# Kernel tuning notes

Measured on AMD Instinct MI355X. Metric: run time of the kernel, lower is better.

The kernel has to match this reference:

```python
import jax, jax.numpy as jnp
import numpy as np

B, L, D, H = 2, 2048, 1024, 16
DK = D // H


def setup_inputs() -> dict:
    key = jax.random.key(0)
    ks = jax.random.split(key, 13)
    s = 1.0 / np.sqrt(D)
    return {
        "q": jax.random.normal(ks[0], (B, L, D), jnp.float32),
        "k": jax.random.normal(ks[1], (B, L, D), jnp.float32),
        "v": jax.random.normal(ks[2], (B, L, D), jnp.float32),
        "mask": jax.random.randint(ks[3], (B, L, L), 0, 2, jnp.int32),
        "Wq": jax.random.normal(ks[4], (D, D), jnp.float32) * s,
        "bq": jnp.zeros((D,), jnp.float32),
        "Wk": jax.random.normal(ks[5], (D, D), jnp.float32) * s,
        "bk": jnp.zeros((D,), jnp.float32),
        "Wv": jax.random.normal(ks[6], (D, D), jnp.float32) * s,
        "bv": jnp.zeros((D,), jnp.float32),
        "Wo": jax.random.normal(ks[7], (D, D), jnp.float32) * s,
        "bo": jnp.zeros((D,), jnp.float32),
    }


def reference(q, k, v, mask, Wq, bq, Wk, bk, Wv, bv, Wo, bo):
    # projections: [B, L, D] -> [B, L, H, DK]
    qh = (q @ Wq + bq).reshape(B, L, H, DK)
    kh = (k @ Wk + bk).reshape(B, L, H, DK)
    vh = (v @ Wv + bv).reshape(B, L, H, DK)
    # scores scaled by d_model (module passes model_dim=d_model, not sqrt(d_k))
    attn = jnp.einsum("bqhd,bkhd->bhqk", qh, kh) / D
    attn = jnp.where(mask[:, None, :, :] == 0, jnp.float32(-1e9), attn)
    attn = jax.nn.softmax(attn, axis=-1)  # [B, H, Lq, Lk]
    ctx = jnp.einsum("bhqk,bkhd->bqhd", attn, vh)  # [B, Lq, H, DK]
    out = ctx.reshape(B, L, D) @ Wo + bo
    # original returns attn flattened head-major: [H*B, Lq, Lk]
    attn_out = attn.transpose(1, 0, 2, 3).reshape(H * B, L, L)
    return out, attn_out
```

## Files before the change

kernel.cpp:

```cpp
#include <hip/hip_runtime.h>
#include <cstdint>

typedef unsigned short u16;
typedef unsigned long long u64;
typedef __attribute__((ext_vector_type(8))) short short8;
typedef __attribute__((ext_vector_type(4))) float floatx4;

#define DEV __device__ __forceinline__

#define GLD16(gp, lp)                                                          \
  __builtin_amdgcn_global_load_lds(                                            \
      (const __attribute__((address_space(1))) void*)(gp),                     \
      (__attribute__((address_space(3))) void*)(lp), 16, 0, 0)

DEV u16 f2bf(float f) {
  union { float f; uint32_t u; } x; x.f = f;
  uint32_t r = x.u + 0x7fffu + ((x.u >> 16) & 1u);
  return (u16)(r >> 16);
}


__global__ __launch_bounds__(256) void cvt_bf16(
    const float* __restrict__ src, u16* __restrict__ dst) {
  int i = (blockIdx.x * 256 + threadIdx.x) * 4;
  float4 v = *(const float4*)(src + i);
  ushort4 o;
  o.x = f2bf(v.x); o.y = f2bf(v.y); o.z = f2bf(v.z); o.w = f2bf(v.w);
  *(ushort4*)(dst + i) = o;
}

__global__ __launch_bounds__(256) void pack_mask(
    const int* __restrict__ mask, u64* __restrict__ mw) {
  const int lane = threadIdx.x & 63;
  int gw = (blockIdx.x * 256 + threadIdx.x) >> 6;
  const int nwaves = (gridDim.x * 256) >> 6;
  const int total = (2 * 2048 * 2048) / 64;
  for (int c = gw; c < total; c += nwaves) {
    int v = mask[(size_t)c * 64 + lane];
    u64 b = __ballot(v != 0);
    if (lane == 0) mw[c] = b;
  }
}

__global__ __launch_bounds__(256) void transpose_w(
    const float* __restrict__ s0, const float* __restrict__ s1,
    const float* __restrict__ s2, const float* __restrict__ s3,
    u16* __restrict__ d0, u16* __restrict__ d1,
    u16* __restrict__ d2, u16* __restrict__ d3) {
  const float* S; u16* D;
  switch (blockIdx.z) {
    case 0: S = s0; D = d0; break;
    case 1: S = s1; D = d1; break;
    case 2: S = s2; D = d2; break;
    default: S = s3; D = d3; break;
  }
  __shared__ u16 t[64][68];
  const int tid = threadIdx.x;
  const int r0 = blockIdx.y * 64, c0 = blockIdx.x * 64;
#pragma unroll
  for (int i = 0; i < 4; ++i) {
    int idx = i * 256 + tid;
    int r = idx >> 4, c = (idx & 15) * 4;
    float4 v = *(const float4*)(S + (size_t)(r0 + r) * 1024 + c0 + c);
    t[r][c] = f2bf(v.x); t[r][c + 1] = f2bf(v.y);
    t[r][c + 2] = f2bf(v.z); t[r][c + 3] = f2bf(v.w);
  }
  __syncthreads();
#pragma unroll
  for (int i = 0; i < 4; ++i) {
    int idx = i * 256 + tid;
    int r = idx >> 4, c = (idx & 15) * 4;
    ushort4 v;
    v.x = t[c][r]; v.y = t[c + 1][r]; v.z = t[c + 2][r]; v.w = t[c + 3][r];
    *(ushort4*)(D + (size_t)(c0 + r) * 1024 + r0 + c) = v;
  }
}

__global__ __launch_bounds__(256) void gemm128(
    const u16* __restrict__ X, const u16* __restrict__ Wt,
    const float* __restrict__ bias, u16* __restrict__ outb,
    float* __restrict__ outf, int mode) {
  __shared__ __align__(16) u16 As[128 * 32];
  __shared__ __align__(16) u16 Bs[128 * 32];
  const int tid = threadIdx.x;
  const int wave = tid >> 6, lane = tid & 63;
  const int quad = lane >> 4, l16 = lane & 15;
  const int wm = (wave >> 1) * 64, wn = (wave & 1) * 64;
  const int m0 = blockIdx.x * 128, n0 = blockIdx.y * 128;

  floatx4 acc[4][4];
#pragma unroll
  for (int i = 0; i < 4; ++i)
#pragma unroll
    for (int j = 0; j < 4; ++j) acc[i][j] = (floatx4){0.f, 0.f, 0.f, 0.f};

  for (int k0 = 0; k0 < 1024; k0 += 32) {
#pragma unroll
    for (int r = 0; r < 2; ++r) {
      int c = r * 256 + tid;
      int row = c >> 2, off = (c & 3) * 8;
      GLD16(X + (size_t)(m0 + row) * 1024 + k0 + off, As + c * 8);
      GLD16(Wt + (size_t)(n0 + row) * 1024 + k0 + off, Bs + c * 8);
    }
    __syncthreads();
    short8 a[4], b[4];
#pragma unroll
    for (int i = 0; i < 4; ++i)
      a[i] = *(const short8*)(As + (wm + i * 16 + l16) * 32 + quad * 8);
#pragma unroll
    for (int i = 0; i < 4; ++i)
      b[i] = *(const short8*)(Bs + (wn + i * 16 + l16) * 32 + quad * 8);
#pragma unroll
    for (int mi = 0; mi < 4; ++mi)
#pragma unroll
      for (int ni = 0; ni < 4; ++ni)
        acc[mi][ni] = __builtin_amdgcn_mfma_f32_16x16x32_bf16(
            a[mi], b[ni], acc[mi][ni], 0, 0, 0);
    __syncthreads();
  }

#pragma unroll
  for (int mi = 0; mi < 4; ++mi) {
#pragma unroll
    for (int ni = 0; ni < 4; ++ni) {
      const int gn = n0 + wn + ni * 16 + l16;
      const float bv = bias[gn];
#pragma unroll
      for (int reg = 0; reg < 4; ++reg) {
        const int gm = m0 + wm + mi * 16 + quad * 4 + reg;
        const float v = acc[mi][ni][reg] + bv;
        if (mode == 2) {
          outf[(size_t)gm * 1024 + gn] = v;
        } else {
          int bb = gm >> 11, l = gm & 2047, hh = gn >> 6, dk = gn & 63;
          size_t addr = (mode == 0)
              ? (((size_t)(bb * 16 + hh) * 2048 + l) * 64 + dk)
              : (((size_t)(bb * 16 + hh) * 64 + dk) * 2048 + l);
          outb[addr] = f2bf(v);
        }
      }
    }
  }
}

__global__ __launch_bounds__(256) void rowsum_k(
    const u16* __restrict__ qh, const u16* __restrict__ kh,
    const u64* __restrict__ mw, float* __restrict__ rowinv) {
  const int tid = threadIdx.x;
  const int wave = tid >> 6, lane = tid & 63;
  const int quad = lane >> 4, l16 = lane & 15;
  const int q0 = blockIdx.x * 64, h = blockIdx.y, b = blockIdx.z;
  const int bh = b * 16 + h;

  __shared__ __align__(16) u16 Qs[64 * 72];
  __shared__ __align__(16) u16 Ks[128 * 72];
  __shared__ float red[4][64];

  const u16* qbase = qh + ((size_t)bh * 2048 + q0) * 64;
  const u16* kbase = kh + (size_t)bh * 2048 * 64;
  const u64* mwrow = mw + ((size_t)b * 2048 + q0) * 32;

#pragma unroll
  for (int r = 0; r < 2; ++r) {
    int c = r * 256 + tid;
    int row = c >> 3, off = (c & 7) * 8;
    uint4 v = *(const uint4*)(qbase + (size_t)c * 8);
    *(uint4*)(Qs + row * 72 + off) = v;
  }

  float rs[4][4];
#pragma unroll
  for (int i = 0; i < 4; ++i)
#pragma unroll
    for (int j = 0; j < 4; ++j) rs[i][j] = 0.f;

  for (int kt = 0; kt < 16; ++kt) {
#pragma unroll
    for (int r = 0; r < 4; ++r) {
      int c = r * 256 + tid;
      int row = c >> 3, off = (c & 7) * 8;
      uint4 v = *(const uint4*)(kbase + (size_t)kt * 8192 + c * 8);
      *(uint4*)(Ks + row * 72 + off) = v;
    }
    __syncthreads();

    floatx4 s[4][2];
#pragma unroll
    for (int i = 0; i < 4; ++i) {
      s[i][0] = (floatx4){0.f, 0.f, 0.f, 0.f};
      s[i][1] = (floatx4){0.f, 0.f, 0.f, 0.f};
    }
#pragma unroll
    for (int kk = 0; kk < 64; kk += 32) {
      short8 a[4], bb[2];
#pragma unroll
      for (int i = 0; i < 4; ++i)
        a[i] = *(const short8*)(Qs + (i * 16 + l16) * 72 + kk + quad * 8);
#pragma unroll
      for (int j = 0; j < 2; ++j)
        bb[j] = *(const short8*)(Ks + (wave * 32 + j * 16 + l16) * 72 + kk + quad * 8);
#pragma unroll
      for (int mi = 0; mi < 4; ++mi)
#pragma unroll
        for (int ni = 0; ni < 2; ++ni)
          s[mi][ni] = __builtin_amdgcn_mfma_f32_16x16x32_bf16(
              a[mi], bb[ni], s[mi][ni], 0, 0, 0);
    }
#pragma unroll
    for (int mi = 0; mi < 4; ++mi)
#pragma unroll
      for (int reg = 0; reg < 4; ++reg) {
        int row = mi * 16 + quad * 4 + reg;
        u64 w = mwrow[row * 32 + kt * 2 + (wave >> 1)];
#pragma unroll
        for (int ni = 0; ni < 2; ++ni) {
          int bit = (wave & 1) * 32 + ni * 16 + l16;
          float sv = s[mi][ni][reg] * (1.0f / 1024.0f);
          rs[mi][reg] += ((w >> bit) & 1) ? __expf(sv) : 0.f;
        }
      }
    __syncthreads();
  }

#pragma unroll
  for (int mi = 0; mi < 4; ++mi)
#pragma unroll
    for (int reg = 0; reg < 4; ++reg) {
      float v = rs[mi][reg];
      v += __shfl_xor(v, 1, 64);
      v += __shfl_xor(v, 2, 64);
      v += __shfl_xor(v, 4, 64);
      v += __shfl_xor(v, 8, 64);
      rs[mi][reg] = v;
    }
  if (l16 == 0) {
#pragma unroll
    for (int mi = 0; mi < 4; ++mi)
#pragma unroll
      for (int reg = 0; reg < 4; ++reg)
        red[wave][mi * 16 + quad * 4 + reg] = rs[mi][reg];
  }
  __syncthreads();
  if (tid < 64) {
    float sum = red[0][tid] + red[1][tid] + red[2][tid] + red[3][tid];
    rowinv[(size_t)bh * 2048 + q0 + tid] = (sum > 0.f) ? (1.0f / sum) : -1.0f;
  }
}

__global__ __launch_bounds__(256) void attn_k(
    const u16* __restrict__ qh, const u16* __restrict__ kh,
    const u16* __restrict__ vt, const u64* __restrict__ mw,
    const float* __restrict__ rowinv, float* __restrict__ attn_out,
    u16* __restrict__ ctx) {
  const int tid = threadIdx.x;
  const int wave = tid >> 6, lane = tid & 63;
  const int quad = lane >> 4, l16 = lane & 15;
  const int q0 = blockIdx.x * 64, h = blockIdx.y, b = blockIdx.z;
  const int bh = b * 16 + h;

  __shared__ __align__(16) u16 Qs[64 * 72];
  __shared__ __align__(16) u16 Ks[128 * 72];
  __shared__ __align__(16) u16 Vs[64 * 136];
  __shared__ __align__(16) u16 Ps[64 * 136];

  const u16* qbase = qh + ((size_t)bh * 2048 + q0) * 64;
  const u16* kbase = kh + (size_t)bh * 2048 * 64;
  const u16* vbase = vt + (size_t)bh * 64 * 2048;
  const u64* mwrow = mw + ((size_t)b * 2048 + q0) * 32;
  float* abase = attn_out + ((size_t)(h * 2 + b) * 2048 + q0) * 2048;

#pragma unroll
  for (int r = 0; r < 2; ++r) {
    int c = r * 256 + tid;
    int row = c >> 3, off = (c & 7) * 8;
    uint4 v = *(const uint4*)(qbase + (size_t)c * 8);
    *(uint4*)(Qs + row * 72 + off) = v;
  }

  float inv[4][4];
#pragma unroll
  for (int mi = 0; mi < 4; ++mi)
#pragma unroll
    for (int reg = 0; reg < 4; ++reg)
      inv[mi][reg] = rowinv[(size_t)bh * 2048 + q0 + mi * 16 + quad * 4 + reg];

  floatx4 cacc[4];
#pragma unroll
  for (int i = 0; i < 4; ++i) cacc[i] = (floatx4){0.f, 0.f, 0.f, 0.f};

  for (int kt = 0; kt < 16; ++kt) {
#pragma unroll
    for (int r = 0; r < 4; ++r) {
      int c = r * 256 + tid;
      int row = c >> 3, off = (c & 7) * 8;
      uint4 v = *(const uint4*)(kbase + (size_t)kt * 8192 + c * 8);
      *(uint4*)(Ks + row * 72 + off) = v;
      int dk = c >> 4, ko = (c & 15) * 8;
      uint4 w = *(const uint4*)(vbase + (size_t)dk * 2048 + kt * 128 + ko);
      *(uint4*)(Vs + dk * 136 + ko) = w;
    }
    __syncthreads();

    floatx4 s[4][2];
#pragma unroll
    for (int i = 0; i < 4; ++i) {
      s[i][0] = (floatx4){0.f, 0.f, 0.f, 0.f};
      s[i][1] = (floatx4){0.f, 0.f, 0.f, 0.f};
    }
#pragma unroll
    for (int kk = 0; kk < 64; kk += 32) {
      short8 a[4], bb[2];
#pragma unroll
      for (int i = 0; i < 4; ++i)
        a[i] = *(const short8*)(Qs + (i * 16 + l16) * 72 + kk + quad * 8);
#pragma unroll
      for (int j = 0; j < 2; ++j)
        bb[j] = *(const short8*)(Ks + (wave * 32 + j * 16 + l16) * 72 + kk + quad * 8);
#pragma unroll
      for (int mi = 0; mi < 4; ++mi)
#pragma unroll
        for (int ni = 0; ni < 2; ++ni)
          s[mi][ni] = __builtin_amdgcn_mfma_f32_16x16x32_bf16(
              a[mi], bb[ni], s[mi][ni], 0, 0, 0);
    }

#pragma unroll
    for (int mi = 0; mi < 4; ++mi)
#pragma unroll
      for (int reg = 0; reg < 4; ++reg) {
        int row = mi * 16 + quad * 4 + reg;
        u64 w = mwrow[row * 32 + kt * 2 + (wave >> 1)];
        float iv = inv[mi][reg];
#pragma unroll
        for (int ni = 0; ni < 2; ++ni) {
          int keyl = wave * 32 + ni * 16 + l16;
          int key = kt * 128 + keyl;
          int bit = (wave & 1) * 32 + ni * 16 + l16;
          float sv = s[mi][ni][reg] * (1.0f / 1024.0f);
          float p = (iv < 0.f) ? (1.0f / 2048.0f)
                               : (((w >> bit) & 1) ? __expf(sv) * iv : 0.f);
          abase[(size_t)row * 2048 + key] = p;
          Ps[row * 136 + keyl] = f2bf(p);
        }
      }
    __syncthreads();

#pragma unroll
    for (int ks = 0; ks < 4; ++ks) {
      short8 a[4];
#pragma unroll
      for (int mi = 0; mi < 4; ++mi)
        a[mi] = *(const short8*)(Ps + (mi * 16 + l16) * 136 + ks * 32 + quad * 8);
      short8 bb = *(const short8*)(Vs + (wave * 16 + l16) * 136 + ks * 32 + quad * 8);
#pragma unroll
      for (int mi = 0; mi < 4; ++mi)
        cacc[mi] = __builtin_amdgcn_mfma_f32_16x16x32_bf16(a[mi], bb, cacc[mi], 0, 0, 0);
    }
    __syncthreads();
  }

#pragma unroll
  for (int mi = 0; mi < 4; ++mi)
#pragma unroll
    for (int reg = 0; reg < 4; ++reg) {
      int row = q0 + mi * 16 + quad * 4 + reg;
      int col = h * 64 + wave * 16 + l16;
      ctx[(size_t)(b * 2048 + row) * 1024 + col] = f2bf(cacc[mi][reg]);
    }
}

extern "C" void kernel_launch(void* const* d_in, const int* in_sizes, int n_in,
                              void* d_out, int out_size, void* d_ws, size_t ws_size,
                              hipStream_t stream) {
  const float* q    = (const float*)d_in[0];
  const float* k    = (const float*)d_in[1];
  const float* v    = (const float*)d_in[2];
  const int*   mask = (const int*)d_in[3];
  const float* Wq   = (const float*)d_in[4];
  const float* bq   = (const float*)d_in[5];
  const float* Wk   = (const float*)d_in[6];
  const float* bk   = (const float*)d_in[7];
  const float* Wv   = (const float*)d_in[8];
  const float* bv   = (const float*)d_in[9];
  const float* Wo   = (const float*)d_in[10];
  const float* bo   = (const float*)d_in[11];

  float* out  = (float*)d_out;
  float* attn = out + (size_t)4096 * 1024;

  const size_t M = 1u << 20;
  u16* wtq = (u16*)d_ws;
  u16* wtk = wtq + M;
  u16* wtv = wtk + M;
  u16* wto = wtv + M;
  u16* xb  = wto + M;
  u16* qh  = xb + 4 * M;
  u16* kh  = qh + 4 * M;
  u16* vt  = kh + 4 * M;
  u16* ctx = xb;
  float* rinv = (float*)(vt + 4 * M);
  u64* mw = (u64*)(rinv + 64 * 1024);

  pack_mask<<<dim3(512), 256, 0, stream>>>(mask, mw);
  transpose_w<<<dim3(16, 16, 4), 256, 0, stream>>>(Wq, Wk, Wv, Wo, wtq, wtk, wtv, wto);

  cvt_bf16<<<dim3(4096), 256, 0, stream>>>(q, xb);
  gemm128<<<dim3(32, 8), 256, 0, stream>>>(xb, wtq, bq, qh, nullptr, 0);
  cvt_bf16<<<dim3(4096), 256, 0, stream>>>(k, xb);
  gemm128<<<dim3(32, 8), 256, 0, stream>>>(xb, wtk, bk, kh, nullptr, 0);
  cvt_bf16<<<dim3(4096), 256, 0, stream>>>(v, xb);
  gemm128<<<dim3(32, 8), 256, 0, stream>>>(xb, wtv, bv, vt, nullptr, 1);

  rowsum_k<<<dim3(32, 16, 2), 256, 0, stream>>>(qh, kh, mw, rinv);
  attn_k<<<dim3(32, 16, 2), 256, 0, stream>>>(qh, kh, vt, mw, rinv, attn, ctx);
  gemm128<<<dim3(32, 8), 256, 0, stream>>>(ctx, wto, bo, nullptr, out, 2);
}
```

Before: 952.2 us.

## Materialize unnormalized bf16 probabilities in first pass and reuse in second

The row-sum pass now also stores the masked exponentials as bf16 to a workspace buffer. The second pass loads them instead of recomputing QK^T and mask bits, normalizes them with vectorized stores into the attention output, and applies the row inverse to the context at the end. This removes the duplicated score GEMM and exp work. In exchange it adds a large extra write and read of the bf16 probability matrix through HBM.

Measured after the change: 988.6 us. 3.8% more time.

```diff
diff --git a/kernel.cpp b/kernel.cpp
--- a/kernel.cpp
+++ b/kernel.cpp
@@ -17,6 +17,10 @@
   union { float f; uint32_t u; } x; x.f = f;
   uint32_t r = x.u + 0x7fffu + ((x.u >> 16) & 1u);
   return (u16)(r >> 16);
+}
+DEV float bf2f(u16 b) {
+  union { uint32_t u; float f; } x; x.u = ((uint32_t)b) << 16;
+  return x.f;
 }
 
 
@@ -143,9 +147,10 @@
   }
 }
 
-__global__ __launch_bounds__(256) void rowsum_k(
+__global__ __launch_bounds__(256) void attn_p1(
     const u16* __restrict__ qh, const u16* __restrict__ kh,
-    const u64* __restrict__ mw, float* __restrict__ rowinv) {
+    const u64* __restrict__ mw, u16* __restrict__ p16,
+    float* __restrict__ rowinv) {
   const int tid = threadIdx.x;
   const int wave = tid >> 6, lane = tid & 63;
   const int quad = lane >> 4, l16 = lane & 15;
@@ -159,6 +164,7 @@
   const u16* qbase = qh + ((size_t)bh * 2048 + q0) * 64;
   const u16* kbase = kh + (size_t)bh * 2048 * 64;
   const u64* mwrow = mw + ((size_t)b * 2048 + q0) * 32;
+  u16* pbase = p16 + ((size_t)bh * 2048 + q0) * 2048;
 
 #pragma unroll
   for (int r = 0; r < 2; ++r) {
@@ -215,8 +221,11 @@
 #pragma unroll
         for (int ni = 0; ni < 2; ++ni) {
           int bit = (wave & 1) * 32 + ni * 16 + l16;
+          int key = kt * 128 + wave * 32 + ni * 16 + l16;
           float sv = s[mi][ni][reg] * (1.0f / 1024.0f);
-          rs[mi][reg] += ((w >> bit) & 1) ? __expf(sv) : 0.f;
+          float e = ((w >> bit) & 1) ? __expf(sv) : 0.f;
+          rs[mi][reg] += e;
+          pbase[(size_t)row * 2048 + key] = f2bf(e);
         }
       }
     __syncthreads();
@@ -247,9 +256,8 @@
   }
 }
 
-__global__ __launch_bounds__(256) void attn_k(
-    const u16* __restrict__ qh, const u16* __restrict__ kh,
-    const u16* __restrict__ vt, const u64* __restrict__ mw,
+__global__ __launch_bounds__(256) void attn_p2(
+    const u16* __restrict__ p16, const u16* __restrict__ vt,
     const float* __restrict__ rowinv, float* __restrict__ attn_out,
     u16* __restrict__ ctx) {
   const int tid = threadIdx.x;
@@ -258,91 +266,54 @@
   const int q0 = blockIdx.x * 64, h = blockIdx.y, b = blockIdx.z;
   const int bh = b * 16 + h;
 
-  __shared__ __align__(16) u16 Qs[64 * 72];
-  __shared__ __align__(16) u16 Ks[128 * 72];
+  __shared__ __align__(16) u16 Ps[64 * 136];
   __shared__ __align__(16) u16 Vs[64 * 136];
-  __shared__ __align__(16) u16 Ps[64 * 136];
-
-  const u16* qbase = qh + ((size_t)bh * 2048 + q0) * 64;
-  const u16* kbase = kh + (size_t)bh * 2048 * 64;
+  __shared__ float inv_s[64];
+
+  const u16* pbase = p16 + ((size_t)bh * 2048 + q0) * 2048;
   const u16* vbase = vt + (size_t)bh * 64 * 2048;
-  const u64* mwrow = mw + ((size_t)b * 2048 + q0) * 32;
   float* abase = attn_out + ((size_t)(h * 2 + b) * 2048 + q0) * 2048;
 
-#pragma unroll
-  for (int r = 0; r < 2; ++r) {
-    int c = r * 256 + tid;
-    int row = c >> 3, off = (c & 7) * 8;
-    uint4 v = *(const uint4*)(qbase + (size_t)c * 8);
-    *(uint4*)(Qs + row * 72 + off) = v;
-  }
-
-  float inv[4][4];
-#pragma unroll
-  for (int mi = 0; mi < 4; ++mi)
-#pragma unroll
-    for (int reg = 0; reg < 4; ++reg)
-      inv[mi][reg] = rowinv[(size_t)bh * 2048 + q0 + mi * 16 + quad * 4 + reg];
+  if (tid < 64) inv_s[tid] = rowinv[(size_t)bh * 2048 + q0 + tid];
 
   floatx4 cacc[4];
 #pragma unroll
   for (int i = 0; i < 4; ++i) cacc[i] = (floatx4){0.f, 0.f, 0.f, 0.f};
+
+  const uint4 pb_unif = {0x3A003A00u, 0x3A003A00u, 0x3A003A00u, 0x3A003A00u};
 
   for (int kt = 0; kt < 16; ++kt) {
 #pragma unroll
     for (int r = 0; r < 4; ++r) {
       int c = r * 256 + tid;
-      int row = c >> 3, off = (c & 7) * 8;
-      uint4 v = *(const uint4*)(kbase + (size_t)kt * 8192 + c * 8);
-      *(uint4*)(Ks + row * 72 + off) = v;
-      int dk = c >> 4, ko = (c & 15) * 8;
-      uint4 w = *(const uint4*)(vbase + (size_t)dk * 2048 + kt * 128 + ko);
-      *(uint4*)(Vs + dk * 136 + ko) = w;
-    }
-    __syncthreads();
-
-    floatx4 s[4][2];
-#pragma unroll
-    for (int i = 0; i < 4; ++i) {
-      s[i][0] = (floatx4){0.f, 0.f, 0.f, 0.f};
-      s[i][1] = (floatx4){0.f, 0.f, 0.f, 0.f};
-    }
-#pragma unroll
-    for (int kk = 0; kk < 64; kk += 32) {
-      short8 a[4], bb[2];
-#pragma unroll
-      for (int i = 0; i < 4; ++i)
-        a[i] = *(const short8*)(Qs + (i * 16 + l16) * 72 + kk + quad * 8);
-#pragma unroll
-      for (int j = 0; j < 2; ++j)
-        bb[j] = *(const short8*)(Ks + (wave * 32 + j * 16 + l16) * 72 + kk + quad * 8);
-#pragma unroll
-      for (int mi = 0; mi < 4; ++mi)
-#pragma unroll
-        for (int ni = 0; ni < 2; ++ni)
-          s[mi][ni] = __builtin_amdgcn_mfma_f32_16x16x32_bf16(
-              a[mi], bb[ni], s[mi][ni], 0, 0, 0);
-    }
-
-#pragma unroll
-    for (int mi = 0; mi < 4; ++mi)
-#pragma unroll
-      for (int reg = 0; reg < 4; ++reg) {
-        int row = mi * 16 + quad * 4 + reg;
-        u64 w = mwrow[row * 32 + kt * 2 + (wave >> 1)];
-        float iv = inv[mi][reg];
-#pragma unroll
-        for (int ni = 0; ni < 2; ++ni) {
-          int keyl = wave * 32 + ni * 16 + l16;
-          int key = kt * 128 + keyl;
-          int bit = (wave & 1) * 32 + ni * 16 + l16;
-          float sv = s[mi][ni][reg] * (1.0f / 1024.0f);
-          float p = (iv < 0.f) ? (1.0f / 2048.0f)
-                               : (((w >> bit) & 1) ? __expf(sv) * iv : 0.f);
-          abase[(size_t)row * 2048 + key] = p;
-          Ps[row * 136 + keyl] = f2bf(p);
-        }
+      int row = c >> 4, ko = (c & 15) * 8;
+      uint4 p = *(const uint4*)(pbase + (size_t)row * 2048 + kt * 128 + ko);
+      *(uint4*)(Ps + row * 136 + ko) = p;
+      uint4 w = *(const uint4*)(vbase + (size_t)row * 2048 + kt * 128 + ko);
+      *(uint4*)(Vs + row * 136 + ko) = w;
+    }
+    __syncthreads();
+
+#pragma unroll
+    for (int r = 0; r < 4; ++r) {
+      int c = r * 256 + tid;
+      int row = c >> 4, ko = (c & 15) * 8;
+      float iv = inv_s[row];
+      uint4 p = *(const uint4*)(Ps + row * 136 + ko);
+      float o[8];
+      if (iv < 0.f) {
+#pragma unroll
+        for (int j = 0; j < 8; ++j) o[j] = 1.0f / 2048.0f;
+        *(uint4*)(Ps + row * 136 + ko) = pb_unif;
+      } else {
+        const u16* pu = (const u16*)&p;
+#pragma unroll
+        for (int j = 0; j < 8; ++j) o[j] = bf2f(pu[j]) * iv;
       }
+      float* dst = abase + (size_t)row * 2048 + kt * 128 + ko;
+      *(float4*)(dst) = (float4){o[0], o[1], o[2], o[3]};
+      *(float4*)(dst + 4) = (float4){o[4], o[5], o[6], o[7]};
+    }
     __syncthreads();
 
 #pragma unroll
@@ -363,9 +334,12 @@
   for (int mi = 0; mi < 4; ++mi)
 #pragma unroll
     for (int reg = 0; reg < 4; ++reg) {
-      int row = q0 + mi * 16 + quad * 4 + reg;
+      int row = mi * 16 + quad * 4 + reg;
+      float iv = inv_s[row];
+      float sc = (iv < 0.f) ? 1.0f : iv;
+      int grow = q0 + row;
       int col = h * 64 + wave * 16 + l16;
-      ctx[(size_t)(b * 2048 + row) * 1024 + col] = f2bf(cacc[mi][reg]);
+      ctx[(size_t)(b * 2048 + grow) * 1024 + col] = f2bf(cacc[mi][reg] * sc);
     }
 }
 
@@ -400,6 +374,7 @@
   u16* ctx = xb;
   float* rinv = (float*)(vt + 4 * M);
   u64* mw = (u64*)(rinv + 64 * 1024);
+  u16* p16 = (u16*)(mw + 131072);
 
   pack_mask<<<dim3(512), 256, 0, stream>>>(mask, mw);
   transpose_w<<<dim3(16, 16, 4), 256, 0, stream>>>(Wq, Wk, Wv, Wo, wtq, wtk, wtv, wto);
@@ -411,7 +386,7 @@
   cvt_bf16<<<dim3(4096), 256, 0, stream>>>(v, xb);
   gemm128<<<dim3(32, 8), 256, 0, stream>>>(xb, wtv, bv, vt, nullptr, 1);
 
-  rowsum_k<<<dim3(32, 16, 2), 256, 0, stream>>>(qh, kh, mw, rinv);
-  attn_k<<<dim3(32, 16, 2), 256, 0, stream>>>(qh, kh, vt, mw, rinv, attn, ctx);
+  attn_p1<<<dim3(32, 16, 2), 256, 0, stream>>>(qh, kh, mw, p16, rinv);
+  attn_p2<<<dim3(32, 16, 2), 256, 0, stream>>>(p16, vt, rinv, attn, ctx);
   gemm128<<<dim3(32, 8), 256, 0, stream>>>(ctx, wto, bo, nullptr, out, 2);
 }
```
